# Performance work log

Measured on AMD Instinct MI355X. Metric: run time of the kernel, lower is better.

Reference implementation:

```python
import jax, jax.numpy as jnp
import numpy as np

HEADS = 16
MAX_SEQ_LEN = 1024
ALPHA = 1.0


def setup_inputs() -> dict:
    key = jax.random.key(0)
    ks = jax.random.split(key, 16)
    b, n, dim = 2, 1024, 1024
    s = 0.02
    x = jax.random.normal(ks[0], (b, n, dim), jnp.float32)
    Wq = jax.random.normal(ks[1], (dim, dim), jnp.float32) * s
    Wk = jax.random.normal(ks[2], (dim, dim), jnp.float32) * s
    Wv = jax.random.normal(ks[3], (dim, dim), jnp.float32) * s
    Wo = jax.random.normal(ks[4], (dim, dim), jnp.float32) * s
    E_idx = jax.random.normal(ks[5], (MAX_SEQ_LEN, HEADS), jnp.float32) * s
    # padding_idx=0 rows zero-initialized (as in torch nn.Embedding(padding_idx=0))
    E_bar = (jax.random.normal(ks[6], (17, HEADS), jnp.float32) * s).at[0].set(0.0)
    E_pos = (jax.random.normal(ks[7], (96, HEADS), jnp.float32) * s).at[0].set(0.0)
    E_oct = (jax.random.normal(ks[8], (25, HEADS), jnp.float32) * s).at[0].set(0.0)
    E_semi = (jax.random.normal(ks[9], (13, HEADS), jnp.float32) * s).at[0].set(0.0)
    # structure matrices: raw values in [0, table_size-2]; forward adds +1
    bar = jax.random.randint(ks[10], (b, n, n), 0, 16, dtype=jnp.int32)
    position = jax.random.randint(ks[11], (b, n, n), 0, 95, dtype=jnp.int32)
    octave = jax.random.randint(ks[12], (b, n, n), 0, 24, dtype=jnp.int32)
    semitone = jax.random.randint(ks[13], (b, n, n), 0, 12, dtype=jnp.int32)
    return {"x": x, "Wq": Wq, "Wk": Wk, "Wv": Wv, "Wo": Wo,
            "E_idx": E_idx, "E_bar": E_bar, "E_pos": E_pos,
            "E_oct": E_oct, "E_semi": E_semi,
            "bar": bar, "position": position, "octave": octave, "semitone": semitone}


def reference(x, Wq, Wk, Wv, Wo, E_idx, E_bar, E_pos, E_oct, E_semi,
              bar, position, octave, semitone):
    b, n, dim = x.shape
    h = HEADS
    d = dim // h

    def split_heads(t):  # (b,n,dim) -> (b,h,n,d)
        return t.reshape(b, n, h, d).transpose(0, 2, 1, 3)

    q = split_heads(x @ Wq.T)
    k = split_heads(x @ Wk.T)
    v = split_heads(x @ Wv.T)

    qk = jnp.einsum('bhid,bhjd->bhij', q, k)

    # relative index bias: (1,h,n,n)
    rel_pos = jnp.clip(jnp.arange(n)[:, None] - jnp.arange(n)[None, :], 0, MAX_SEQ_LEN - 1)
    srel = E_idx[rel_pos].transpose(2, 0, 1)[None]

    # structure biases: embedding lookups -> (b,h,n,n)
    s_time = (E_bar[bar + 1] + E_pos[position + 1]).transpose(0, 3, 1, 2)
    s_pitch = (E_oct[octave + 1] + E_semi[semitone + 1]).transpose(0, 3, 1, 2)

    dots = (qk + ALPHA * (srel + s_time + s_pitch)) / jnp.sqrt(jnp.float32(d))

    causal_mask = jnp.triu(jnp.ones((n, n), dtype=bool), k=1)
    mask_value = -jnp.finfo(dots.dtype).max
    dots = jnp.where(causal_mask, mask_value, dots)

    attn = jax.nn.softmax(dots, axis=-1)  # dropout=0 at eval
    out = jnp.einsum('bhij,bhjd->bhid', attn, v)
    out = out.transpose(0, 2, 1, 3).reshape(b, n, dim)
    return out @ Wo.T
```

## Files before the change

### kernel.cpp

```cpp
#include <hip/hip_runtime.h>
#include <cstdint>
#include <math.h>

typedef __attribute__((ext_vector_type(8))) short short8;
typedef __attribute__((ext_vector_type(4))) float f32x4;

#define LOG2E 1.44269504088896340736f

static __device__ __forceinline__ float bf2f(unsigned short u) {
    union { unsigned int i; float f; } v; v.i = ((unsigned int)u) << 16; return v.f;
}
static __device__ __forceinline__ unsigned short f2bf(float f) {
    union { float f; unsigned int i; } v; v.f = f;
    unsigned int r = v.i + 0x7FFF + ((v.i >> 16) & 1);
    return (unsigned short)(r >> 16);
}

__global__ __launch_bounds__(256) void k_prep(
    const float* __restrict__ x, const float* __restrict__ wq,
    const float* __restrict__ wk, const float* __restrict__ wv,
    const float* __restrict__ wo, unsigned short* __restrict__ dstconv,
    const float* __restrict__ Eidx, const float* __restrict__ Ebar,
    const float* __restrict__ Epos, const float* __restrict__ Eoct,
    const float* __restrict__ Esemi,
    const int* __restrict__ barm, const int* __restrict__ posm,
    const int* __restrict__ octm, const int* __restrict__ semim,
    unsigned short* __restrict__ biasg) {
    __shared__ float2 t2[8 * 233];
    __shared__ int    pk[16 * 65];

    if (blockIdx.x >= 1088) {
        long t = (long)(blockIdx.x - 1088) * 256 + threadIdx.x;
        long base = t * 4;
        const long NX = 2097152, NW = 1048576;
        const float* src; long off;
        if (base < NX)            { src = x;  off = base; }
        else if (base < NX + NW)  { src = wq; off = base - NX; }
        else if (base < NX + 2*NW){ src = wk; off = base - NX - NW; }
        else if (base < NX + 3*NW){ src = wv; off = base - NX - 2*NW; }
        else                      { src = wo; off = base - NX - 3*NW; }
        float4 v = *(const float4*)(src + off);
        ushort4 o;
        o.x = f2bf(v.x); o.y = f2bf(v.y); o.z = f2bf(v.z); o.w = f2bf(v.w);
        *(ushort4*)(dstconv + base) = o;
        return;
    }
    int fid = blockIdx.x;
    int b = (fid >= 544) ? 1 : 0;
    int f = fid - b * 544;
    int ti, tj;
    if (f >= 480) { int rr = f - 480; ti = 60 + (rr >> 4); tj = rr & 15; }
    else {
        int g = (int)(0.5f * (sqrtf(1.0f + 2.0f * (float)f) - 1.0f));
        while (2 * (g + 1) * (g + 2) <= f) g++;
        while (2 * g * (g + 1) > f) g--;
        int rr = f - 2 * g * (g + 1);
        int q = rr / (g + 1);
        ti = g * 4 + q;
        tj = rr - q * (g + 1);
    }
    int i0 = ti * 16, j0 = tj * 64;

    int t = threadIdx.x;
    int rel_lo = i0 - j0 - 63; if (rel_lo < 0) rel_lo = 0;

    for (int idx = t; idx < 231 * 8; idx += 256) {
        int s = idx >> 3, h2 = idx & 7;
        float va, vb;
        if (s < 80) {
            int src = rel_lo + s; if (src > 1023) src = 1023;
            va = Eidx[src * 16 + h2]; vb = Eidx[src * 16 + h2 + 8];
        } else if (s < 97)  { va = Ebar[(s - 80) * 16 + h2];  vb = Ebar[(s - 80) * 16 + h2 + 8]; }
        else if (s < 193)   { va = Epos[(s - 97) * 16 + h2];  vb = Epos[(s - 97) * 16 + h2 + 8]; }
        else if (s < 218)   { va = Eoct[(s - 193) * 16 + h2]; vb = Eoct[(s - 193) * 16 + h2 + 8]; }
        else                { va = Esemi[(s - 218) * 16 + h2]; vb = Esemi[(s - 218) * 16 + h2 + 8]; }
        t2[h2 * 233 + s] = make_float2(va, vb);
    }
    #pragma unroll
    for (int cc = 0; cc < 4; cc++) {
        int cell = t + cc * 256;
        int i = i0 + (cell >> 6), j = j0 + (cell & 63);
        long ij = ((long)b << 20) + ((long)i << 10) + j;
        int v = (barm[ij] + 1) | ((posm[ij] + 1) << 5) |
                ((octm[ij] + 1) << 12) | ((semim[ij] + 1) << 17);
        pk[(cell >> 6) * 65 + (cell & 63)] = v;
    }
    __syncthreads();

    int lane = t & 63, q = t & 15, G = (t >> 4) & 3, hq = t >> 6;
    int base_rel = (i0 + q) - j0 - rel_lo;
    const float2* TA = &t2[hq * 233];
    const float2* TB = &t2[(hq + 4) * 233];
    long tbase = ((((long)(b * 16) * 64 + ti) * 16 + tj) << 10) + lane * 16;
    #pragma unroll
    for (int sub = 0; sub < 4; sub++) {
        ushort4 o0, o1, o2, o3;
        #pragma unroll
        for (int rr = 0; rr < 4; rr++) {
            int key = sub * 16 + G * 4 + rr;
            int p = pk[q * 65 + key];
            int sr = base_rel - key; if (sr < 0) sr = 0;
            float2 a0 = TA[sr];
            float2 a1 = TA[80  + (p & 31)];
            float2 a2 = TA[97  + ((p >> 5)  & 127)];
            float2 a3 = TA[193 + ((p >> 12) & 31)];
            float2 a4 = TA[218 + ((p >> 17) & 15)];
            float2 b0 = TB[sr];
            float2 b1 = TB[80  + (p & 31)];
            float2 b2 = TB[97  + ((p >> 5)  & 127)];
            float2 b3 = TB[193 + ((p >> 12) & 31)];
            float2 b4 = TB[218 + ((p >> 17) & 15)];
            float xA = a0.x + a1.x + a2.x + a3.x + a4.x;
            float yA = a0.y + a1.y + a2.y + a3.y + a4.y;
            float xB = b0.x + b1.x + b2.x + b3.x + b4.x;
            float yB = b0.y + b1.y + b2.y + b3.y + b4.y;
            ((unsigned short*)&o0)[rr] = f2bf(xA * 0.125f);
            ((unsigned short*)&o1)[rr] = f2bf(xB * 0.125f);
            ((unsigned short*)&o2)[rr] = f2bf(yA * 0.125f);
            ((unsigned short*)&o3)[rr] = f2bf(yB * 0.125f);
        }
        *(ushort4*)(biasg + tbase + ((long)hq        << 20) + sub * 4) = o0;
        *(ushort4*)(biasg + tbase + ((long)(hq + 4)  << 20) + sub * 4) = o1;
        *(ushort4*)(biasg + tbase + ((long)(hq + 8)  << 20) + sub * 4) = o2;
        *(ushort4*)(biasg + tbase + ((long)(hq + 12) << 20) + sub * 4) = o3;
    }
}

__global__ __launch_bounds__(256) void k_gemm(
    const unsigned short* __restrict__ A,
    const unsigned short* __restrict__ B0, const unsigned short* __restrict__ B1,
    const unsigned short* __restrict__ B2,
    unsigned short* __restrict__ qd, unsigned short* __restrict__ kd,
    unsigned short* __restrict__ vtd, float* __restrict__ outf, int mode) {
    __shared__ unsigned short As[128 * 64];
    __shared__ unsigned short Bs[64 * 64];
    int md = (mode < 0) ? (int)blockIdx.z : mode;
    const unsigned short* B = (md == 1) ? B1 : (md == 2) ? B2 : B0;
    int m0 = blockIdx.x * 128, n0 = blockIdx.y * 64;
    int t = threadIdx.x;
    int w = t >> 6, lane = t & 63, g = lane >> 4, c = lane & 15;
    int wr = w >> 1, wc = w & 1;
    const int K = 1024;
    f32x4 zero = {0.f, 0.f, 0.f, 0.f};
    f32x4 acc[4][2];
    #pragma unroll
    for (int m = 0; m < 4; m++)
        #pragma unroll
        for (int n = 0; n < 2; n++) acc[m][n] = zero;

    int srow = w * 8 + (lane >> 3);
    int scol = (lane & 7) * 8;
    for (int k0 = 0; k0 < K; k0 += 64) {
        __syncthreads();
        #pragma unroll
        for (int qq = 0; qq < 4; qq++) {
            int row = qq * 32 + srow;
            __builtin_amdgcn_global_load_lds(
                (const __attribute__((address_space(1))) unsigned int*)(A + (long)(m0 + row) * K + k0 + scol),
                (__attribute__((address_space(3))) unsigned int*)&As[(qq * 32 + w * 8) * 64],
                16, 0, 0);
        }
        #pragma unroll
        for (int qq = 0; qq < 2; qq++) {
            int row = qq * 32 + srow;
            __builtin_amdgcn_global_load_lds(
                (const __attribute__((address_space(1))) unsigned int*)(B + (long)(n0 + row) * K + k0 + scol),
                (__attribute__((address_space(3))) unsigned int*)&Bs[(qq * 32 + w * 8) * 64],
                16, 0, 0);
        }
        __syncthreads();
        #pragma unroll
        for (int kk = 0; kk < 2; kk++) {
            short8 a[4], bb[2];
            #pragma unroll
            for (int m = 0; m < 4; m++)
                a[m] = *(const short8*)&As[(wr * 64 + m * 16 + c) * 64 + kk * 32 + g * 8];
            #pragma unroll
            for (int n = 0; n < 2; n++)
                bb[n] = *(const short8*)&Bs[(wc * 32 + n * 16 + c) * 64 + kk * 32 + g * 8];
            #pragma unroll
            for (int m = 0; m < 4; m++)
                #pragma unroll
                for (int n = 0; n < 2; n++)
                    acc[m][n] = __builtin_amdgcn_mfma_f32_16x16x32_bf16(a[m], bb[n], acc[m][n], 0, 0, 0);
        }
    }

    if (md <= 1) {
        unsigned short* dst = (md == 0) ? qd : kd;
        float scale = (md == 0) ? 0.125f : 1.0f;
        #pragma unroll
        for (int m = 0; m < 4; m++) {
            #pragma unroll
            for (int r = 0; r < 4; r++) {
                int mm = m0 + wr * 64 + m * 16 + g * 4 + r;
                int bb2 = mm >> 10, ii = mm & 1023;
                #pragma unroll
                for (int n = 0; n < 2; n++) {
                    int nn = n0 + wc * 32 + n * 16 + c;
                    int hh = nn >> 6, dd = nn & 63;
                    dst[(((long)(bb2 * 16 + hh) << 10) + ii) * 64 + dd] = f2bf(acc[m][n][r] * scale);
                }
            }
        }
    } else if (md == 2) {
        #pragma unroll
        for (int m = 0; m < 4; m++) {
            int mm0 = m0 + wr * 64 + m * 16 + g * 4;
            int bb2 = mm0 >> 10, ii = mm0 & 1023;
            #pragma unroll
            for (int n = 0; n < 2; n++) {
                int nn = n0 + wc * 32 + n * 16 + c;
                int hh = nn >> 6, dd = nn & 63;
                ushort4 pkv;
                pkv.x = f2bf(acc[m][n][0]); pkv.y = f2bf(acc[m][n][1]);
                pkv.z = f2bf(acc[m][n][2]); pkv.w = f2bf(acc[m][n][3]);
                *(ushort4*)&vtd[(((long)(bb2 * 16 + hh) << 6) + dd) * 1024 + ii] = pkv;
            }
        }
    } else {
        #pragma unroll
        for (int m = 0; m < 4; m++) {
            #pragma unroll
            for (int r = 0; r < 4; r++) {
                long mm = m0 + wr * 64 + m * 16 + g * 4 + r;
                #pragma unroll
                for (int n = 0; n < 2; n++) {
                    int nn = n0 + wc * 32 + n * 16 + c;
                    outf[mm * 1024 + nn] = acc[m][n][r];
                }
            }
        }
    }
}

#define LOADT(KA, KB, BV, JT) do {                                             \
    int _j0 = (JT) * 64;                                                       \
    _Pragma("unroll")                                                          \
    for (int _s = 0; _s < 4; _s++) {                                           \
        const unsigned short* _kr = Kp + (long)(_j0 + _s * 16 + c) * 64 + g * 8; \
        KA[_s] = *(const short8*)(_kr);                                        \
        KB[_s] = *(const short8*)(_kr + 32);                                   \
    }                                                                          \
    const unsigned short* _bp = Bt + ((JT) << 10) + lane * 16;                 \
    BV[0] = *(const short8*)(_bp);                                             \
    BV[1] = *(const short8*)(_bp + 8);                                         \
} while (0)

#define BODY(KA, KB, BV, JT) do {                                             \
    int _j0 = (JT) * 64;                                                      \
    f32x4 _s[4];                                                              \
    _Pragma("unroll")                                                         \
    for (int _sub = 0; _sub < 4; _sub++) {                                    \
        _s[_sub] = __builtin_amdgcn_mfma_f32_16x16x32_bf16(KA[_sub], q0, zero, 0, 0, 0); \
        _s[_sub] = __builtin_amdgcn_mfma_f32_16x16x32_bf16(KB[_sub], q1, _s[_sub], 0, 0, 0); \
    }                                                                         \
    short8 _v0[4], _v1[4];                                                    \
    _Pragma("unroll")                                                         \
    for (int _dd = 0; _dd < 4; _dd++) {                                       \
        const unsigned short* _vb = Vp + (long)(_dd * 16 + c) * 1024 + _j0 + g * 8; \
        _v0[_dd] = *(const short8*)(_vb);                                     \
        _v1[_dd] = *(const short8*)(_vb + 32);                                \
    }                                                                         \
    unsigned int _P0[4], _P1[4];                                              \
    _Pragma("unroll")                                                         \
    for (int _sub = 0; _sub < 4; _sub++) {                                    \
        float _pe[4];                                                         \
        _Pragma("unroll")                                                     \
        for (int _r = 0; _r < 4; _r++) {                                      \
            int _idx = _sub * 4 + _r;                                         \
            float _ss = _s[_sub][_r] +                                        \
                ((_idx < 8) ? bf2f((unsigned short)BV[0][_idx])               \
                            : bf2f((unsigned short)BV[1][_idx - 8]));         \
            if ((JT) == nj - 1 && _j0 + _sub * 16 + g * 4 + _r > i0 + c)      \
                _ss = -1e9f;                                                  \
            _pe[_r] = exp2f(__builtin_fmaf(_ss, LOG2E, -8.0f * LOG2E));       \
            l += _pe[_r];                                                     \
        }                                                                     \
        asm("v_cvt_pk_bf16_f32 %0, %1, %2" : "=v"(_P0[_sub]) : "v"(_pe[0]), "v"(_pe[1])); \
        asm("v_cvt_pk_bf16_f32 %0, %1, %2" : "=v"(_P1[_sub]) : "v"(_pe[2]), "v"(_pe[3])); \
    }                                                                         \
    _Pragma("unroll")                                                         \
    for (int _ch = 0; _ch < 2; _ch++) {                                       \
        unsigned int _a0 = (unsigned int)__shfl((int)_P0[_ch * 2],     srcA); \
        unsigned int _a1 = (unsigned int)__shfl((int)_P0[_ch * 2 + 1], srcA); \
        unsigned int _b0 = (unsigned int)__shfl((int)_P1[_ch * 2],     srcA); \
        unsigned int _b1 = (unsigned int)__shfl((int)_P1[_ch * 2 + 1], srcA); \
        unsigned int _c0 = (unsigned int)__shfl((int)_P0[_ch * 2],     srcB); \
        unsigned int _c1 = (unsigned int)__shfl((int)_P0[_ch * 2 + 1], srcB); \
        unsigned int _d0 = (unsigned int)__shfl((int)_P1[_ch * 2],     srcB); \
        unsigned int _d1 = (unsigned int)__shfl((int)_P1[_ch * 2 + 1], srcB); \
        union { unsigned int u[4]; short8 s8; } _pb;                          \
        _pb.u[0] = sel ? _a1 : _a0;                                           \
        _pb.u[1] = sel ? _b1 : _b0;                                           \
        _pb.u[2] = sel ? _c1 : _c0;                                           \
        _pb.u[3] = sel ? _d1 : _d0;                                           \
        _Pragma("unroll")                                                     \
        for (int _dd = 0; _dd < 4; _dd++)                                     \
            o[_dd] = __builtin_amdgcn_mfma_f32_16x16x32_bf16(                 \
                (_ch == 0) ? _v0[_dd] : _v1[_dd], _pb.s8, o[_dd], 0, 0, 0);   \
    }                                                                         \
} while (0)

__global__ __launch_bounds__(256) void k_attn(
    const unsigned short* __restrict__ Qs, const unsigned short* __restrict__ Ks,
    const unsigned short* __restrict__ VTs, const unsigned short* __restrict__ biasg,
    unsigned short* __restrict__ Os) {
    int bid = blockIdx.x;
    int itg = (bid < 256) ? (15 - (bid >> 5)) : ((bid - 256) >> 5);
    int bh = bid & 31;
    int b = bh >> 4, h = bh & 15;
    int w = threadIdx.x >> 6;
    int lane = threadIdx.x & 63;
    int g = lane >> 4, c = lane & 15;
    int it = itg * 4 + w;
    int i0 = it * 16;
    int srcA = ((lane >> 4) & 1) * 32 + c;
    int srcB = srcA + 16;
    int sel  = (lane >> 5) & 1;

    long plane = ((long)bh) << 16;
    const unsigned short* Qp = Qs + plane;
    const unsigned short* Kp = Ks + plane;
    const unsigned short* Vp = VTs + plane;
    const unsigned short* Bt = biasg + (((long)bh * 64 + it) << 14);

    short8 q0 = *(const short8*)(Qp + (long)(i0 + c) * 64 + g * 8);
    short8 q1 = *(const short8*)(Qp + (long)(i0 + c) * 64 + 32 + g * 8);

    f32x4 zero = {0.f, 0.f, 0.f, 0.f};
    f32x4 o[4]; o[0] = zero; o[1] = zero; o[2] = zero; o[3] = zero;
    float l = 0.f;

    int nj = itg + 1;
    short8 kaA[4], kbA[4], bvA[2];
    short8 kaB[4], kbB[4], bvB[2];
    LOADT(kaA, kbA, bvA, 0);
    for (int jt = 0; jt < nj; jt += 2) {
        if (jt + 1 < nj) LOADT(kaB, kbB, bvB, jt + 1);
        BODY(kaA, kbA, bvA, jt);
        if (jt + 1 < nj) {
            if (jt + 2 < nj) LOADT(kaA, kbA, bvA, jt + 2);
            BODY(kaB, kbB, bvB, jt + 1);
        }
    }
    float lv = l;
    lv += __shfl_xor(lv, 16);
    lv += __shfl_xor(lv, 32);
    float linv = 1.0f / lv;
    int i = i0 + c;
    unsigned short* op = Os + ((long)(b * 1024 + i)) * 1024 + h * 64 + g * 4;
    #pragma unroll
    for (int db = 0; db < 4; db++) {
        ushort4 o4;
        o4.x = f2bf(o[db][0] * linv); o4.y = f2bf(o[db][1] * linv);
        o4.z = f2bf(o[db][2] * linv); o4.w = f2bf(o[db][3] * linv);
        *(ushort4*)(op + db * 16) = o4;
    }
}

extern "C" void kernel_launch(void* const* d_in, const int* in_sizes, int n_in,
                              void* d_out, int out_size, void* d_ws, size_t ws_size,
                              hipStream_t stream) {
    const float* x     = (const float*)d_in[0];
    const float* Wq    = (const float*)d_in[1];
    const float* Wk    = (const float*)d_in[2];
    const float* Wv    = (const float*)d_in[3];
    const float* Wo    = (const float*)d_in[4];
    const float* Eidx  = (const float*)d_in[5];
    const float* Ebar  = (const float*)d_in[6];
    const float* Epos  = (const float*)d_in[7];
    const float* Eoct  = (const float*)d_in[8];
    const float* Esemi = (const float*)d_in[9];
    const int* barm    = (const int*)d_in[10];
    const int* posm    = (const int*)d_in[11];
    const int* octm    = (const int*)d_in[12];
    const int* semim   = (const int*)d_in[13];
    float* outf = (float*)d_out;

    unsigned short* w = (unsigned short*)d_ws;
    unsigned short* XB   = w;
    unsigned short* WQB  = w + 2097152;
    unsigned short* WKB  = w + 3145728;
    unsigned short* WVB  = w + 4194304;
    unsigned short* WOB  = w + 5242880;
    unsigned short* QS   = w + 6291456;
    unsigned short* KS   = w + 8388608;
    unsigned short* VTS  = w + 10485760;
    unsigned short* OS   = w + 12582912;
    unsigned short* BIAS = w + 14680064;

    k_prep<<<7232, 256, 0, stream>>>(x, Wq, Wk, Wv, Wo, w,
                                     Eidx, Ebar, Epos, Eoct, Esemi,
                                     barm, posm, octm, semim, BIAS);
    k_gemm<<<dim3(16, 16, 3), 256, 0, stream>>>(XB, WQB, WKB, WVB,
                                                QS, KS, VTS, nullptr, -1);
    k_attn<<<512, 256, 0, stream>>>(QS, KS, VTS, BIAS, OS);
    k_gemm<<<dim3(16, 16, 1), 256, 0, stream>>>(OS, WOB, WOB, WOB,
                                                QS, KS, VTS, outf, 3);
}
```

Baseline: 100.5 us.

## Overlap bias precompute with QKV projection GEMM in one fused launch

The fp32-to-bf16 conversion now runs as its own kernel. The QKV projection GEMM blocks are merged into the same launch as the bias-table precompute blocks, so the memory-bound bias gather can run alongside the compute-bound GEMM on different CUs. This also drops one kernel launch boundary. The cost is a larger shared-memory footprint per block for the union of both roles, which may lower occupancy for the bias blocks.

```diff
diff --git a/kernel.cpp b/kernel.cpp
--- a/kernel.cpp
+++ b/kernel.cpp
@@ -16,35 +16,133 @@
     return (unsigned short)(r >> 16);
 }
 
-__global__ __launch_bounds__(256) void k_prep(
+__global__ __launch_bounds__(256) void k_convert(
     const float* __restrict__ x, const float* __restrict__ wq,
     const float* __restrict__ wk, const float* __restrict__ wv,
-    const float* __restrict__ wo, unsigned short* __restrict__ dstconv,
+    const float* __restrict__ wo, unsigned short* __restrict__ dst) {
+    long t = (long)blockIdx.x * 256 + threadIdx.x;
+    long base = t * 4;
+    const long NX = 2097152, NW = 1048576;
+    const float* src; long off;
+    if (base < NX)            { src = x;  off = base; }
+    else if (base < NX + NW)  { src = wq; off = base - NX; }
+    else if (base < NX + 2*NW){ src = wk; off = base - NX - NW; }
+    else if (base < NX + 3*NW){ src = wv; off = base - NX - 2*NW; }
+    else                      { src = wo; off = base - NX - 3*NW; }
+    float4 v = *(const float4*)(src + off);
+    ushort4 o;
+    o.x = f2bf(v.x); o.y = f2bf(v.y); o.z = f2bf(v.z); o.w = f2bf(v.w);
+    *(ushort4*)(dst + base) = o;
+}
+
+__global__ __launch_bounds__(256) void k_fuse(
+    const unsigned short* __restrict__ A,
+    const unsigned short* __restrict__ B0, const unsigned short* __restrict__ B1,
+    const unsigned short* __restrict__ B2,
+    unsigned short* __restrict__ qd, unsigned short* __restrict__ kd,
+    unsigned short* __restrict__ vtd,
     const float* __restrict__ Eidx, const float* __restrict__ Ebar,
     const float* __restrict__ Epos, const float* __restrict__ Eoct,
     const float* __restrict__ Esemi,
     const int* __restrict__ barm, const int* __restrict__ posm,
     const int* __restrict__ octm, const int* __restrict__ semim,
     unsigned short* __restrict__ biasg) {
-    __shared__ float2 t2[8 * 233];
-    __shared__ int    pk[16 * 65];
+    __shared__ char smem[24576];
+    int t = threadIdx.x;
 
     if (blockIdx.x >= 1088) {
-        long t = (long)(blockIdx.x - 1088) * 256 + threadIdx.x;
-        long base = t * 4;
-        const long NX = 2097152, NW = 1048576;
-        const float* src; long off;
-        if (base < NX)            { src = x;  off = base; }
-        else if (base < NX + NW)  { src = wq; off = base - NX; }
-        else if (base < NX + 2*NW){ src = wk; off = base - NX - NW; }
-        else if (base < NX + 3*NW){ src = wv; off = base - NX - 2*NW; }
-        else                      { src = wo; off = base - NX - 3*NW; }
-        float4 v = *(const float4*)(src + off);
-        ushort4 o;
-        o.x = f2bf(v.x); o.y = f2bf(v.y); o.z = f2bf(v.z); o.w = f2bf(v.w);
-        *(ushort4*)(dstconv + base) = o;
+        unsigned short* As = (unsigned short*)smem;
+        unsigned short* Bs = (unsigned short*)(smem + 16384);
+        int gid = blockIdx.x - 1088;
+        int md = gid >> 8;
+        int bx = gid & 15, by = (gid >> 4) & 15;
+        const unsigned short* B = (md == 1) ? B1 : (md == 2) ? B2 : B0;
+        int m0 = bx * 128, n0 = by * 64;
+        int w = t >> 6, lane = t & 63, g = lane >> 4, c = lane & 15;
+        int wr = w >> 1, wc = w & 1;
+        const int K = 1024;
+        f32x4 zero = {0.f, 0.f, 0.f, 0.f};
+        f32x4 acc[4][2];
+        #pragma unroll
+        for (int m = 0; m < 4; m++)
+            #pragma unroll
+            for (int n = 0; n < 2; n++) acc[m][n] = zero;
+
+        int srow = w * 8 + (lane >> 3);
+        int scol = (lane & 7) * 8;
+        for (int k0 = 0; k0 < K; k0 += 64) {
+            __syncthreads();
+            #pragma unroll
+            for (int qq = 0; qq < 4; qq++) {
+                int row = qq * 32 + srow;
+                __builtin_amdgcn_global_load_lds(
+                    (const __attribute__((address_space(1))) unsigned int*)(A + (long)(m0 + row) * K + k0 + scol),
+                    (__attribute__((address_space(3))) unsigned int*)&As[(qq * 32 + w * 8) * 64],
+                    16, 0, 0);
+            }
+            #pragma unroll
+            for (int qq = 0; qq < 2; qq++) {
+                int row = qq * 32 + srow;
+                __builtin_amdgcn_global_load_lds(
+                    (const __attribute__((address_space(1))) unsigned int*)(B + (long)(n0 + row) * K + k0 + scol),
+                    (__attribute__((address_space(3))) unsigned int*)&Bs[(qq * 32 + w * 8) * 64],
+                    16, 0, 0);
+            }
+            __syncthreads();
+            #pragma unroll
+            for (int kk = 0; kk < 2; kk++) {
+                short8 a[4], bb[2];
+                #pragma unroll
+                for (int m = 0; m < 4; m++)
+                    a[m] = *(const short8*)&As[(wr * 64 + m * 16 + c) * 64 + kk * 32 + g * 8];
+                #pragma unroll
+                for (int n = 0; n < 2; n++)
+                    bb[n] = *(const short8*)&Bs[(wc * 32 + n * 16 + c) * 64 + kk * 32 + g * 8];
+                #pragma unroll
+                for (int m = 0; m < 4; m++)
+                    #pragma unroll
+                    for (int n = 0; n < 2; n++)
+                        acc[m][n] = __builtin_amdgcn_mfma_f32_16x16x32_bf16(a[m], bb[n], acc[m][n], 0, 0, 0);
+            }
+        }
+
+        if (md <= 1) {
+            unsigned short* dst = (md == 0) ? qd : kd;
+            float scale = (md == 0) ? 0.125f : 1.0f;
+            #pragma unroll
+            for (int m = 0; m < 4; m++) {
+                #pragma unroll
+                for (int r = 0; r < 4; r++) {
+                    int mm = m0 + wr * 64 + m * 16 + g * 4 + r;
+                    int bb2 = mm >> 10, ii = mm & 1023;
+                    #pragma unroll
+                    for (int n = 0; n < 2; n++) {
+                        int nn = n0 + wc * 32 + n * 16 + c;
+                        int hh = nn >> 6, dd = nn & 63;
+                        dst[(((long)(bb2 * 16 + hh) << 10) + ii) * 64 + dd] = f2bf(acc[m][n][r] * scale);
+                    }
+                }
+            }
+        } else {
+            #pragma unroll
+            for (int m = 0; m < 4; m++) {
+                int mm0 = m0 + wr * 64 + m * 16 + g * 4;
+                int bb2 = mm0 >> 10, ii = mm0 & 1023;
+                #pragma unroll
+                for (int n = 0; n < 2; n++) {
+                    int nn = n0 + wc * 32 + n * 16 + c;
+                    int hh = nn >> 6, dd = nn & 63;
+                    ushort4 pkv;
+                    pkv.x = f2bf(acc[m][n][0]); pkv.y = f2bf(acc[m][n][1]);
+                    pkv.z = f2bf(acc[m][n][2]); pkv.w = f2bf(acc[m][n][3]);
+                    *(ushort4*)&vtd[(((long)(bb2 * 16 + hh) << 6) + dd) * 1024 + ii] = pkv;
+                }
+            }
+        }
         return;
     }
+    float2* t2 = (float2*)smem;
+    int*    pk = (int*)(smem + 14912);
     int fid = blockIdx.x;
     int b = (fid >= 544) ? 1 : 0;
     int f = fid - b * 544;
@@ -60,8 +158,6 @@
         tj = rr - q * (g + 1);
     }
     int i0 = ti * 16, j0 = tj * 64;
-
-    int t = threadIdx.x;
     int rel_lo = i0 - j0 - 63; if (rel_lo < 0) rel_lo = 0;
 
     for (int idx = t; idx < 231 * 8; idx += 256) {
@@ -128,14 +224,10 @@
 
 __global__ __launch_bounds__(256) void k_gemm(
     const unsigned short* __restrict__ A,
-    const unsigned short* __restrict__ B0, const unsigned short* __restrict__ B1,
-    const unsigned short* __restrict__ B2,
-    unsigned short* __restrict__ qd, unsigned short* __restrict__ kd,
-    unsigned short* __restrict__ vtd, float* __restrict__ outf, int mode) {
+    const unsigned short* __restrict__ B0,
+    float* __restrict__ outf) {
     __shared__ unsigned short As[128 * 64];
     __shared__ unsigned short Bs[64 * 64];
-    int md = (mode < 0) ? (int)blockIdx.z : mode;
-    const unsigned short* B = (md == 1) ? B1 : (md == 2) ? B2 : B0;
     int m0 = blockIdx.x * 128, n0 = blockIdx.y * 64;
     int t = threadIdx.x;
     int w = t >> 6, lane = t & 63, g = lane >> 4, c = lane & 15;
@@ -164,7 +256,7 @@
         for (int qq = 0; qq < 2; qq++) {
             int row = qq * 32 + srow;
             __builtin_amdgcn_global_load_lds(
-                (const __attribute__((address_space(1))) unsigned int*)(B + (long)(n0 + row) * K + k0 + scol),
+                (const __attribute__((address_space(1))) unsigned int*)(B0 + (long)(n0 + row) * K + k0 + scol),
                 (__attribute__((address_space(3))) unsigned int*)&Bs[(qq * 32 + w * 8) * 64],
                 16, 0, 0);
         }
@@ -186,49 +278,15 @@
         }
     }
 
-    if (md <= 1) {
-        unsigned short* dst = (md == 0) ? qd : kd;
-        float scale = (md == 0) ? 0.125f : 1.0f;
-        #pragma unroll
-        for (int m = 0; m < 4; m++) {
-            #pragma unroll
-            for (int r = 0; r < 4; r++) {
-                int mm = m0 + wr * 64 + m * 16 + g * 4 + r;
-                int bb2 = mm >> 10, ii = mm & 1023;
-                #pragma unroll
-                for (int n = 0; n < 2; n++) {
-                    int nn = n0 + wc * 32 + n * 16 + c;
-                    int hh = nn >> 6, dd = nn & 63;
-                    dst[(((long)(bb2 * 16 + hh) << 10) + ii) * 64 + dd] = f2bf(acc[m][n][r] * scale);
-                }
-            }
-        }
-    } else if (md == 2) {
-        #pragma unroll
-        for (int m = 0; m < 4; m++) {
-            int mm0 = m0 + wr * 64 + m * 16 + g * 4;
-            int bb2 = mm0 >> 10, ii = mm0 & 1023;
+    #pragma unroll
+    for (int m = 0; m < 4; m++) {
+        #pragma unroll
+        for (int r = 0; r < 4; r++) {
+            long mm = m0 + wr * 64 + m * 16 + g * 4 + r;
             #pragma unroll
             for (int n = 0; n < 2; n++) {
                 int nn = n0 + wc * 32 + n * 16 + c;
-                int hh = nn >> 6, dd = nn & 63;
-                ushort4 pkv;
-                pkv.x = f2bf(acc[m][n][0]); pkv.y = f2bf(acc[m][n][1]);
-                pkv.z = f2bf(acc[m][n][2]); pkv.w = f2bf(acc[m][n][3]);
-                *(ushort4*)&vtd[(((long)(bb2 * 16 + hh) << 6) + dd) * 1024 + ii] = pkv;
-            }
-        }
-    } else {
-        #pragma unroll
-        for (int m = 0; m < 4; m++) {
-            #pragma unroll
-            for (int r = 0; r < 4; r++) {
-                long mm = m0 + wr * 64 + m * 16 + g * 4 + r;
-                #pragma unroll
-                for (int n = 0; n < 2; n++) {
-                    int nn = n0 + wc * 32 + n * 16 + c;
-                    outf[mm * 1024 + nn] = acc[m][n][r];
-                }
+                outf[mm * 1024 + nn] = acc[m][n][r];
             }
         }
     }
@@ -390,12 +448,10 @@
     unsigned short* OS   = w + 12582912;
     unsigned short* BIAS = w + 14680064;
 
-    k_prep<<<7232, 256, 0, stream>>>(x, Wq, Wk, Wv, Wo, w,
+    k_convert<<<6144, 256, 0, stream>>>(x, Wq, Wk, Wv, Wo, w);
+    k_fuse<<<1856, 256, 0, stream>>>(XB, WQB, WKB, WVB, QS, KS, VTS,
                                      Eidx, Ebar, Epos, Eoct, Esemi,
                                      barm, posm, octm, semim, BIAS);
-    k_gemm<<<dim3(16, 16, 3), 256, 0, stream>>>(XB, WQB, WKB, WVB,
-                                                QS, KS, VTS, nullptr, -1);
     k_attn<<<512, 256, 0, stream>>>(QS, KS, VTS, BIAS, OS);
-    k_gemm<<<dim3(16, 16, 1), 256, 0, stream>>>(OS, WOB, WOB, WOB,
-                                                QS, KS, VTS, outf, 3);
-}
+    k_gemm<<<dim3(16, 16), 256, 0, stream>>>(OS, WOB, outf);
+}
```

New measurement: 104.2 us. 1.04x slower.
